# Kernel tuning notes

Hardware: AMD Instinct MI355X
Metric: run time of the kernel (lower is better)

Reference implementation:

```python
import jax, jax.numpy as jnp
import numpy as np

N, F_IN, E, H, C, B = 50000, 128, 800000, 64, 10, 512


def gcn_conv(x, W, b, src, dst, n):
    # PyG GCNConv: h = xW; add self-loops; norm = d^-1/2[src]*d^-1/2[dst]; scatter-add; + bias
    h = x @ W
    deg = jax.ops.segment_sum(jnp.ones(src.shape[0], h.dtype), dst, num_segments=n) + 1.0  # +1 self-loop
    dinv = jax.lax.rsqrt(deg)
    msg = h[src] * (dinv[src] * dinv[dst])[:, None]            # [E, H] gather + scale
    out = jax.ops.segment_sum(msg, dst, num_segments=n)        # scatter-add over targets
    out = out + h * (dinv * dinv)[:, None]                      # self-loop term (norm = 1/deg)
    return out + b


def setup_inputs() -> dict:
    key = jax.random.key(0)
    ks = jax.random.split(key, 12)
    x = jax.random.normal(ks[0], (N, F_IN), dtype=jnp.float32)
    edge_index = jax.random.randint(ks[1], (2, E), 0, N)
    batch = jnp.sort(jax.random.randint(ks[2], (N,), 0, B))
    def glorot(k, fan_in, fan_out):
        s = np.sqrt(6.0 / (fan_in + fan_out)).astype(np.float32)
        return jax.random.uniform(k, (fan_in, fan_out), jnp.float32, -s, s)
    return {
        "x": x, "edge_index": edge_index, "batch": batch,
        "W1": glorot(ks[3], F_IN, H), "b1": jnp.zeros((H,), jnp.float32),
        "W2": glorot(ks[4], H, H),    "b2": jnp.zeros((H,), jnp.float32),
        "W3": glorot(ks[5], H, H),    "b3": jnp.zeros((H,), jnp.float32),
        "Wl": glorot(ks[6], H, C),    "bl": jnp.zeros((C,), jnp.float32),
    }


def reference(x, edge_index, batch, W1, b1, W2, b2, W3, b3, Wl, bl):
    src, dst = edge_index[0], edge_index[1]
    n = x.shape[0]
    h = jax.nn.relu(gcn_conv(x, W1, b1, src, dst, n))
    h = jax.nn.relu(gcn_conv(h, W2, b2, src, dst, n))
    h = gcn_conv(h, W3, b3, src, dst, n)
    # global mean pool over graphs
    sums = jax.ops.segment_sum(h, batch, num_segments=B)
    cnts = jax.ops.segment_sum(jnp.ones((n,), h.dtype), batch, num_segments=B)
    pooled = sums / jnp.maximum(cnts, 1.0)[:, None]
    # dropout is identity in eval mode
    return pooled @ Wl + bl
```

## Files before the change

### kernel.cpp

```cpp
#include <hip/hip_runtime.h>

#define NBSHIFT 8
#define MAXB    5120
#define CHUNK   4096
#define TPB     256

__device__ inline unsigned short f2bf(float f) {
    unsigned u = __builtin_bit_cast(unsigned, f);
    unsigned r = u + 0x7FFFu + ((u >> 16) & 1u);
    return (unsigned short)(r >> 16);
}
__device__ inline float bflo(unsigned u) { return __builtin_bit_cast(float, u << 16); }
__device__ inline float bfhi(unsigned u) { return __builtin_bit_cast(float, u & 0xFFFF0000u); }

__global__ void k_init(int* __restrict__ bcur, int NB) {
    int t = threadIdx.x;
    if (t < NB) bcur[t] = 0;
}

__global__ __launch_bounds__(TPB) void k_bin_seg(const int* __restrict__ src,
                                                 const int* __restrict__ dst,
                                                 int* __restrict__ bcur,
                                                 unsigned* __restrict__ pairbuf,
                                                 const int* __restrict__ batch,
                                                 int* __restrict__ segs,
                                                 int* __restrict__ sege,
                                                 int E, int N, int B, int NB,
                                                 int nbChunk) {
    __shared__ int sdst[CHUNK];
    __shared__ int lcnt[256];
    __shared__ int lbase[256];
    int t = threadIdx.x;
    if ((int)blockIdx.x < nbChunk) {
        int e0 = blockIdx.x * CHUNK;
        int n = min(e0 + CHUNK, E) - e0;
        lcnt[t] = 0;
        __syncthreads();
        for (int i = t; i < n; i += TPB) {
            int d = dst[e0 + i];
            sdst[i] = d;
            atomicAdd(&lcnt[d >> NBSHIFT], 1);
        }
        __syncthreads();
        if (t < NB) {
            int c = lcnt[t];
            lbase[t] = c ? atomicAdd(&bcur[t], c) : 0;
            lcnt[t] = 0;
        }
        __syncthreads();
        for (int i = t; i < n; i += TPB) {
            int d = sdst[i];
            int b = d >> NBSHIFT;
            int pos = lbase[b] + atomicAdd(&lcnt[b], 1);
            pairbuf[(size_t)b * MAXB + pos] =
                ((unsigned)(d & 255) << 24) | (unsigned)src[e0 + i];
        }
    } else {
        int g = ((int)blockIdx.x - nbChunk) * TPB + t;
        if (g < B) {
            int lo = 0, hi = N;
            while (lo < hi) { int m = (lo + hi) >> 1; if (batch[m] < g) lo = m + 1; else hi = m; }
            int s = lo;
            lo = s; hi = N;
            while (lo < hi) { int m = (lo + hi) >> 1; if (batch[m] < g + 1) lo = m + 1; else hi = m; }
            segs[g] = s;
            sege[g] = lo;
        }
    }
}

template <int KHALVES>
__device__ void gemm_tile(const float* __restrict__ in, const float* __restrict__ W,
                          const float* __restrict__ sc, unsigned short* __restrict__ outb,
                          int tile, int N, float* sf) {
    float* sX = sf;
    float* sW = sf + 4096;
    const int K = KHALVES * 64;
    int t = threadIdx.x, w = t >> 6, l = t & 63;
    int node0 = tile * 64;
    int fg = l & 15, ngl = w * 4 + (l >> 4);
    float4 a0 = make_float4(0.f, 0.f, 0.f, 0.f), a1 = a0, a2 = a0, a3 = a0;

    for (int h = 0; h < KHALVES; ++h) {
        __syncthreads();
        for (int i = t; i < 64 * 16; i += TPB)
            ((float4*)sW)[i] = ((const float4*)(W + h * 64 * 64))[i];
        {
            int node = node0 + l;
            bool ok = node < N;
            const float* rp = in + (size_t)node * K + h * 64;
            for (int k0 = w * 16; k0 < w * 16 + 16; k0 += 4) {
                float4 v = ok ? *(const float4*)(rp + k0) : make_float4(0.f, 0.f, 0.f, 0.f);
                sX[(k0 + 0) * 64 + l] = v.x;
                sX[(k0 + 1) * 64 + l] = v.y;
                sX[(k0 + 2) * 64 + l] = v.z;
                sX[(k0 + 3) * 64 + l] = v.w;
            }
        }
        __syncthreads();
#pragma unroll 8
        for (int k = 0; k < 64; ++k) {
            float4 xv = *(const float4*)(sX + k * 64 + ngl * 4);
            float4 wv = *(const float4*)(sW + k * 64 + fg * 4);
            a0.x += xv.x * wv.x; a0.y += xv.x * wv.y; a0.z += xv.x * wv.z; a0.w += xv.x * wv.w;
            a1.x += xv.y * wv.x; a1.y += xv.y * wv.y; a1.z += xv.y * wv.z; a1.w += xv.y * wv.w;
            a2.x += xv.z * wv.x; a2.y += xv.z * wv.y; a2.z += xv.z * wv.z; a2.w += xv.z * wv.w;
            a3.x += xv.w * wv.x; a3.y += xv.w * wv.y; a3.z += xv.w * wv.z; a3.w += xv.w * wv.w;
        }
    }
    int nbase = node0 + ngl * 4;
    float4 accs[4] = {a0, a1, a2, a3};
#pragma unroll
    for (int i = 0; i < 4; ++i) {
        int n = nbase + i;
        if (n < N) {
            float s = sc ? sc[n] : 1.0f;
            float4 o = accs[i];
            ushort4 ob;
            ob.x = f2bf(o.x * s); ob.y = f2bf(o.y * s);
            ob.z = f2bf(o.z * s); ob.w = f2bf(o.w * s);
            *(ushort4*)(outb + (size_t)n * 64 + fg * 4) = ob;
        }
    }
}

__global__ __launch_bounds__(TPB) void k_build_gemm1(const unsigned* __restrict__ pairbuf,
                                                     const int* __restrict__ bcur,
                                                     int* __restrict__ pofs,
                                                     float* __restrict__ dinv,
                                                     int* __restrict__ ssrc,
                                                     const float* __restrict__ x,
                                                     const float* __restrict__ W1,
                                                     unsigned short* __restrict__ hsb,
                                                     int N, int NB) {
    __shared__ __align__(16) float sf[8192];
    int* si = (int*)sf;
    int t = threadIdx.x;
    int bid = blockIdx.x;
    if (bid < NB) {
        int* hcnt = si;
        int* sd   = si + 256;
        int* hcur = si + 512;
        size_t s0 = (size_t)bid * MAXB;
        int cb = bcur[bid];
        hcnt[t] = 0;
        __syncthreads();
        for (int i = t; i < cb; i += TPB)
            atomicAdd(&hcnt[pairbuf[s0 + i] >> 24], 1);
        __syncthreads();
        int c = hcnt[t];
        sd[t] = c;
        __syncthreads();
        int sum = c;
        for (int d = 1; d < 256; d <<= 1) {
            int a = (t >= d) ? sd[t - d] : 0;
            __syncthreads();
            sum += a; sd[t] = sum;
            __syncthreads();
        }
        int excl = sum - c;
        int node = (bid << NBSHIFT) + t;
        if (node < N) {
            pofs[node] = (excl << 8) | c;
            dinv[node] = rsqrtf((float)c + 1.0f);
        }
        hcur[t] = excl;
        __syncthreads();
        for (int i = t; i < cb; i += TPB) {
            unsigned p = pairbuf[s0 + i];
            int pos = atomicAdd(&hcur[p >> 24], 1);
            ssrc[s0 + pos] = (int)(p & 0x00FFFFFFu);
        }
    } else {
        gemm_tile<2>(x, W1, nullptr, hsb, bid - NB, N, sf);
    }
}

template <bool EDGEDINV, bool RELU>
__device__ float4 agg_row(const unsigned short* __restrict__ hs,
                          const int* __restrict__ ssrc, const int* __restrict__ pofs,
                          const float* __restrict__ dinv, const float* __restrict__ bias,
                          int v) {
    int lane = threadIdx.x & 63, g = lane >> 4, fl = lane & 15;
    int pk = pofs[v];
    size_t start = (size_t)(v >> NBSHIFT) * MAXB + (pk >> 8);
    int cnt = pk & 255;
    float dv = dinv[v];
    float4 acc = make_float4(0.f, 0.f, 0.f, 0.f);
#define BF_ACCS(p, s)                                                          \
    do {                                                                       \
        acc.x += bflo((p).x) * (s); acc.y += bfhi((p).x) * (s);                \
        acc.z += bflo((p).y) * (s); acc.w += bfhi((p).y) * (s);                \
    } while (0)
    if (g == 0) {
        uint2 p = *(const uint2*)(hs + (size_t)v * 64 + fl * 4);
        float sc = EDGEDINV ? dv : 1.0f;
        BF_ACCS(p, sc);
    }
    int j = 0, cnt16 = cnt & ~15;
    for (; j < cnt16; j += 16) {
        int s0 = ssrc[start + j + g];
        int s1 = ssrc[start + j + 4 + g];
        int s2 = ssrc[start + j + 8 + g];
        int s3 = ssrc[start + j + 12 + g];
        float d0 = 1.f, d1 = 1.f, d2 = 1.f, d3 = 1.f;
        if (EDGEDINV) { d0 = dinv[s0]; d1 = dinv[s1]; d2 = dinv[s2]; d3 = dinv[s3]; }
        uint2 h0 = *(const uint2*)(hs + (size_t)s0 * 64 + fl * 4);
        uint2 h1 = *(const uint2*)(hs + (size_t)s1 * 64 + fl * 4);
        uint2 h2 = *(const uint2*)(hs + (size_t)s2 * 64 + fl * 4);
        uint2 h3 = *(const uint2*)(hs + (size_t)s3 * 64 + fl * 4);
        BF_ACCS(h0, d0); BF_ACCS(h1, d1); BF_ACCS(h2, d2); BF_ACCS(h3, d3);
    }
    int cnt4 = cnt & ~3;
    for (; j < cnt4; j += 4) {
        int s = ssrc[start + j + g];
        float d = EDGEDINV ? dinv[s] : 1.f;
        uint2 h = *(const uint2*)(hs + (size_t)s * 64 + fl * 4);
        BF_ACCS(h, d);
    }
    int rem = cnt - cnt4;
    if (g < rem) {
        int s = ssrc[start + cnt4 + g];
        float d = EDGEDINV ? dinv[s] : 1.f;
        uint2 h = *(const uint2*)(hs + (size_t)s * 64 + fl * 4);
        BF_ACCS(h, d);
    }
#undef BF_ACCS
    acc.x += __shfl_xor(acc.x, 16); acc.y += __shfl_xor(acc.y, 16);
    acc.z += __shfl_xor(acc.z, 16); acc.w += __shfl_xor(acc.w, 16);
    acc.x += __shfl_xor(acc.x, 32); acc.y += __shfl_xor(acc.y, 32);
    acc.z += __shfl_xor(acc.z, 32); acc.w += __shfl_xor(acc.w, 32);
    float4 bv = *(const float4*)(bias + fl * 4);
    float4 o;
    o.x = acc.x * dv + bv.x; o.y = acc.y * dv + bv.y;
    o.z = acc.z * dv + bv.z; o.w = acc.w * dv + bv.w;
    if (RELU) {
        o.x = fmaxf(o.x, 0.f); o.y = fmaxf(o.y, 0.f);
        o.z = fmaxf(o.z, 0.f); o.w = fmaxf(o.w, 0.f);
    }
    return o;
}

template <bool EDGEDINV>
__global__ __launch_bounds__(512) void k_agg_gemm_tile(const unsigned short* __restrict__ hs,
                                                       const int* __restrict__ ssrc,
                                                       const int* __restrict__ pofs,
                                                       const float* __restrict__ dinv,
                                                       const float* __restrict__ bias,
                                                       const float* __restrict__ W,
                                                       unsigned short* __restrict__ outb,
                                                       int N) {
    __shared__ float sX[64 * 64];
    __shared__ float sW[64 * 64];
    int t = threadIdx.x, w = t >> 6, l = t & 63;
    int g = l >> 4, fl = l & 15;
    for (int i = t; i < 64 * 16; i += 512)
        ((float4*)sW)[i] = ((const float4*)W)[i];
    int node0 = blockIdx.x * 64;
#pragma unroll 2
    for (int i = 0; i < 8; ++i) {
        int nl = w * 8 + i;
        int v = node0 + nl;
        if (v < N) {
            float4 row = agg_row<EDGEDINV, true>(hs, ssrc, pofs, dinv, bias, v);
            if (g == 0) {
                sX[(fl * 4 + 0) * 64 + nl] = row.x;
                sX[(fl * 4 + 1) * 64 + nl] = row.y;
                sX[(fl * 4 + 2) * 64 + nl] = row.z;
                sX[(fl * 4 + 3) * 64 + nl] = row.w;
            }
        }
    }
    __syncthreads();
    int ng = w * 4 + g;
    float4 a0 = make_float4(0.f, 0.f, 0.f, 0.f), a1 = a0;
#pragma unroll 8
    for (int k = 0; k < 64; ++k) {
        float2 xv = *(const float2*)(sX + k * 64 + ng * 2);
        float4 wv = *(const float4*)(sW + k * 64 + fl * 4);
        a0.x += xv.x * wv.x; a0.y += xv.x * wv.y; a0.z += xv.x * wv.z; a0.w += xv.x * wv.w;
        a1.x += xv.y * wv.x; a1.y += xv.y * wv.y; a1.z += xv.y * wv.z; a1.w += xv.y * wv.w;
    }
    int n0 = node0 + ng * 2;
    if (n0 < N) {
        float s = dinv[n0];
        ushort4 ob;
        ob.x = f2bf(a0.x * s); ob.y = f2bf(a0.y * s);
        ob.z = f2bf(a0.z * s); ob.w = f2bf(a0.w * s);
        *(ushort4*)(outb + (size_t)n0 * 64 + fl * 4) = ob;
    }
    if (n0 + 1 < N) {
        float s = dinv[n0 + 1];
        ushort4 ob;
        ob.x = f2bf(a1.x * s); ob.y = f2bf(a1.y * s);
        ob.z = f2bf(a1.z * s); ob.w = f2bf(a1.w * s);
        *(ushort4*)(outb + (size_t)(n0 + 1) * 64 + fl * 4) = ob;
    }
}

__global__ __launch_bounds__(TPB) void k_agg3(const unsigned short* __restrict__ hs,
                                              const int* __restrict__ ssrc,
                                              const int* __restrict__ pofs,
                                              const float* __restrict__ dinv,
                                              const float* __restrict__ bias,
                                              float* __restrict__ outp, int N) {
    int t = threadIdx.x;
    int wave = t >> 6, lane = t & 63;
    int g = lane >> 4, fl = lane & 15;
    int v = blockIdx.x * 4 + wave;
    if (v >= N) return;
    float4 o = agg_row<false, false>(hs, ssrc, pofs, dinv, bias, v);
    if (g == 0)
        *(float4*)(outp + (size_t)v * 64 + fl * 4) = o;
}

__global__ __launch_bounds__(64) void k_pool_classify(const float* __restrict__ h,
                                                      const int* __restrict__ ss,
                                                      const int* __restrict__ se,
                                                      const float* __restrict__ Wl,
                                                      const float* __restrict__ bl,
                                                      float* __restrict__ out, int C) {
    int b = blockIdx.x;
    int lane = threadIdx.x;
    int g = lane >> 4, fl = lane & 15;
    int s = ss[b], e = se[b];
    float4 acc = make_float4(0.f, 0.f, 0.f, 0.f);
#pragma unroll 2
    for (int v = s + g; v < e; v += 4) {
        float4 hv = *(const float4*)(h + (size_t)v * 64 + fl * 4);
        acc.x += hv.x; acc.y += hv.y; acc.z += hv.z; acc.w += hv.w;
    }
    acc.x += __shfl_xor(acc.x, 16); acc.y += __shfl_xor(acc.y, 16);
    acc.z += __shfl_xor(acc.z, 16); acc.w += __shfl_xor(acc.w, 16);
    acc.x += __shfl_xor(acc.x, 32); acc.y += __shfl_xor(acc.y, 32);
    acc.z += __shfl_xor(acc.z, 32); acc.w += __shfl_xor(acc.w, 32);
    if (g == 0) {
        int cnt = e - s;
        if (cnt < 1) cnt = 1;
        float inv = 1.0f / (float)cnt;
        float4 p;
        p.x = acc.x * inv; p.y = acc.y * inv; p.z = acc.z * inv; p.w = acc.w * inv;
        int f0 = fl * 4;
        for (int c = 0; c < C; ++c) {
            float tt = p.x * Wl[(f0 + 0) * C + c] + p.y * Wl[(f0 + 1) * C + c]
                     + p.z * Wl[(f0 + 2) * C + c] + p.w * Wl[(f0 + 3) * C + c];
            tt += __shfl_xor(tt, 1); tt += __shfl_xor(tt, 2);
            tt += __shfl_xor(tt, 4); tt += __shfl_xor(tt, 8);
            if (fl == 0) out[b * C + c] = tt + bl[c];
        }
    }
}


extern "C" void kernel_launch(void* const* d_in, const int* in_sizes, int n_in,
                              void* d_out, int out_size, void* d_ws, size_t ws_size,
                              hipStream_t stream) {
    const float* x    = (const float*)d_in[0];
    const int*   ei   = (const int*)d_in[1];
    const int*   batch= (const int*)d_in[2];
    const float* W1   = (const float*)d_in[3];
    const float* b1   = (const float*)d_in[4];
    const float* W2   = (const float*)d_in[5];
    const float* b2   = (const float*)d_in[6];
    const float* W3   = (const float*)d_in[7];
    const float* b3   = (const float*)d_in[8];
    const float* Wl   = (const float*)d_in[9];
    const float* bl   = (const float*)d_in[10];
    float* out = (float*)d_out;

    const int N = in_sizes[2];
    const int E = in_sizes[1] / 2;
    const int C = 10;
    const int B = out_size / C;
    const int NB = (N + (1 << NBSHIFT) - 1) >> NBSHIFT;
    const int nbChunk = (E + CHUNK - 1) / CHUNK;
    const int nbSeg = (B + TPB - 1) / TPB;
    const int ntiles = (N + 63) / 64;

    char* ws = (char*)d_ws;
    auto alloc = [&](size_t bytes) {
        char* p = ws;
        ws += (bytes + 255) & ~(size_t)255;
        return p;
    };
    int*   bcur = (int*)alloc((size_t)NB * 4);
    int*   segs = (int*)alloc((size_t)B * 4);
    int*   sege = (int*)alloc((size_t)B * 4);
    int*   pofs = (int*)alloc((size_t)N * 4);
    float* dinv = (float*)alloc((size_t)N * 4);
    int*   ssrc = (int*)alloc((size_t)NB * MAXB * 4);
    unsigned short* hsb  = (unsigned short*)alloc((size_t)N * 64 * 2);
    unsigned short* hsb2 = (unsigned short*)alloc((size_t)N * 64 * 2);
    float* act  = (float*)alloc((size_t)N * 64 * 4);
    unsigned* pairbuf = (unsigned*)act;

    const int* src = ei;
    const int* dst = ei + E;

    int gAgg = (N + 3) / 4;

    k_init<<<1, TPB, 0, stream>>>(bcur, NB);
    k_bin_seg<<<nbChunk + nbSeg, TPB, 0, stream>>>(src, dst, bcur, pairbuf,
                                                   batch, segs, sege, E, N, B, NB, nbChunk);
    k_build_gemm1<<<NB + ntiles, TPB, 0, stream>>>(pairbuf, bcur, pofs, dinv, ssrc,
                                                   x, W1, hsb, N, NB);
    k_agg_gemm_tile<true><<<ntiles, 512, 0, stream>>>(hsb, ssrc, pofs, dinv, b1, W2, hsb2, N);
    k_agg_gemm_tile<false><<<ntiles, 512, 0, stream>>>(hsb2, ssrc, pofs, dinv, b2, W3, hsb, N);
    k_agg3<<<gAgg, TPB, 0, stream>>>(hsb, ssrc, pofs, dinv, b3, act, N);
    k_pool_classify<<<B, 64, 0, stream>>>(act, segs, sege, Wl, bl, out, C);
}
```

Baseline: 150.7 us.

## Fuse final aggregation with mean-pool via atomics and shrink binning chunk

The third-layer aggregation is fused with graph pooling. Each wave aggregates 8 consecutive nodes, accumulates rows belonging to the same graph, and atomically adds partial sums into a zeroed pooled buffer. This removes the N×64 fp32 activation write and its re-read by a separate pool kernel, and a small head kernel then does the classifier. The edge-binning chunk size also drops from 4096 to 1024 to launch more blocks, and pairbuf gets its own allocation instead of aliasing the activation buffer. In exchange, the fused path adds float atomic contention and makes the pooled sums order-nondeterministic.

```diff
diff --git a/kernel.cpp b/kernel.cpp
--- a/kernel.cpp
+++ b/kernel.cpp
@@ -2,7 +2,7 @@
 
 #define NBSHIFT 8
 #define MAXB    5120
-#define CHUNK   4096
+#define CHUNK   1024
 #define TPB     256
 
 __device__ inline unsigned short f2bf(float f) {
@@ -13,9 +13,14 @@
 __device__ inline float bflo(unsigned u) { return __builtin_bit_cast(float, u << 16); }
 __device__ inline float bfhi(unsigned u) { return __builtin_bit_cast(float, u & 0xFFFF0000u); }
 
-__global__ void k_init(int* __restrict__ bcur, int NB) {
-    int t = threadIdx.x;
-    if (t < NB) bcur[t] = 0;
+__global__ void k_init(int* __restrict__ bcur, float* __restrict__ pooled,
+                       int NB, int PF) {
+    int bid = blockIdx.x, t = threadIdx.x;
+    if (bid == 0 && t < NB) bcur[t] = 0;
+    if (bid >= 1) {
+        int i = (bid - 1) * TPB + t;
+        if (i < PF) pooled[i] = 0.f;
+    }
 }
 
 __global__ __launch_bounds__(TPB) void k_bin_seg(const int* __restrict__ src,
@@ -298,56 +303,58 @@
     }
 }
 
-__global__ __launch_bounds__(TPB) void k_agg3(const unsigned short* __restrict__ hs,
-                                              const int* __restrict__ ssrc,
-                                              const int* __restrict__ pofs,
-                                              const float* __restrict__ dinv,
-                                              const float* __restrict__ bias,
-                                              float* __restrict__ outp, int N) {
-    int t = threadIdx.x;
-    int wave = t >> 6, lane = t & 63;
-    int g = lane >> 4, fl = lane & 15;
-    int v = blockIdx.x * 4 + wave;
-    if (v >= N) return;
-    float4 o = agg_row<false, false>(hs, ssrc, pofs, dinv, bias, v);
-    if (g == 0)
-        *(float4*)(outp + (size_t)v * 64 + fl * 4) = o;
-}
-
-__global__ __launch_bounds__(64) void k_pool_classify(const float* __restrict__ h,
-                                                      const int* __restrict__ ss,
-                                                      const int* __restrict__ se,
-                                                      const float* __restrict__ Wl,
-                                                      const float* __restrict__ bl,
-                                                      float* __restrict__ out, int C) {
-    int b = blockIdx.x;
-    int lane = threadIdx.x;
-    int g = lane >> 4, fl = lane & 15;
-    int s = ss[b], e = se[b];
-    float4 acc = make_float4(0.f, 0.f, 0.f, 0.f);
-#pragma unroll 2
-    for (int v = s + g; v < e; v += 4) {
-        float4 hv = *(const float4*)(h + (size_t)v * 64 + fl * 4);
-        acc.x += hv.x; acc.y += hv.y; acc.z += hv.z; acc.w += hv.w;
-    }
-    acc.x += __shfl_xor(acc.x, 16); acc.y += __shfl_xor(acc.y, 16);
-    acc.z += __shfl_xor(acc.z, 16); acc.w += __shfl_xor(acc.w, 16);
-    acc.x += __shfl_xor(acc.x, 32); acc.y += __shfl_xor(acc.y, 32);
-    acc.z += __shfl_xor(acc.z, 32); acc.w += __shfl_xor(acc.w, 32);
-    if (g == 0) {
-        int cnt = e - s;
-        if (cnt < 1) cnt = 1;
-        float inv = 1.0f / (float)cnt;
-        float4 p;
-        p.x = acc.x * inv; p.y = acc.y * inv; p.z = acc.z * inv; p.w = acc.w * inv;
-        int f0 = fl * 4;
-        for (int c = 0; c < C; ++c) {
-            float tt = p.x * Wl[(f0 + 0) * C + c] + p.y * Wl[(f0 + 1) * C + c]
-                     + p.z * Wl[(f0 + 2) * C + c] + p.w * Wl[(f0 + 3) * C + c];
-            tt += __shfl_xor(tt, 1); tt += __shfl_xor(tt, 2);
-            tt += __shfl_xor(tt, 4); tt += __shfl_xor(tt, 8);
-            if (fl == 0) out[b * C + c] = tt + bl[c];
-        }
+__global__ __launch_bounds__(512) void k_agg3_pool(const unsigned short* __restrict__ hs,
+                                                   const int* __restrict__ ssrc,
+                                                   const int* __restrict__ pofs,
+                                                   const float* __restrict__ dinv,
+                                                   const float* __restrict__ bias,
+                                                   const int* __restrict__ batch,
+                                                   float* __restrict__ pooled, int N) {
+    int t = threadIdx.x, w = t >> 6, l = t & 63;
+    int g = l >> 4;
+    int node0 = blockIdx.x * 64 + w * 8;
+    float4 pacc = make_float4(0.f, 0.f, 0.f, 0.f);
+    int curg = -1;
+    for (int i = 0; i < 8; ++i) {
+        int v = node0 + i;
+        if (v >= N) break;
+        float4 row = agg_row<false, false>(hs, ssrc, pofs, dinv, bias, v);
+        int gid = batch[v];
+        if (gid != curg) {
+            if (curg >= 0) {
+                float comp = (g == 0) ? pacc.x : (g == 1) ? pacc.y : (g == 2) ? pacc.z : pacc.w;
+                atomicAdd(&pooled[curg * 64 + (l & 15) * 4 + g], comp);
+            }
+            curg = gid;
+            pacc = row;
+        } else {
+            pacc.x += row.x; pacc.y += row.y; pacc.z += row.z; pacc.w += row.w;
+        }
+    }
+    if (curg >= 0) {
+        float comp = (g == 0) ? pacc.x : (g == 1) ? pacc.y : (g == 2) ? pacc.z : pacc.w;
+        atomicAdd(&pooled[curg * 64 + (l & 15) * 4 + g], comp);
+    }
+}
+
+__global__ __launch_bounds__(TPB) void k_head(const float* __restrict__ pooled,
+                                              const int* __restrict__ ss,
+                                              const int* __restrict__ se,
+                                              const float* __restrict__ Wl,
+                                              const float* __restrict__ bl,
+                                              float* __restrict__ out, int B, int C) {
+    int t = threadIdx.x, w = t >> 6, l = t & 63;
+    int b = blockIdx.x * 4 + w;
+    if (b >= B) return;
+    int cnt = se[b] - ss[b];
+    if (cnt < 1) cnt = 1;
+    float p = pooled[b * 64 + l] / (float)cnt;
+    for (int c = 0; c < C; ++c) {
+        float tt = p * Wl[l * C + c];
+        tt += __shfl_xor(tt, 1);  tt += __shfl_xor(tt, 2);
+        tt += __shfl_xor(tt, 4);  tt += __shfl_xor(tt, 8);
+        tt += __shfl_xor(tt, 16); tt += __shfl_xor(tt, 32);
+        if (l == 0) out[b * C + c] = tt + bl[c];
     }
 }
 
@@ -376,6 +383,7 @@
     const int nbChunk = (E + CHUNK - 1) / CHUNK;
     const int nbSeg = (B + TPB - 1) / TPB;
     const int ntiles = (N + 63) / 64;
+    const int PF = B * 64;
 
     char* ws = (char*)d_ws;
     auto alloc = [&](size_t bytes) {
@@ -383,29 +391,27 @@
         ws += (bytes + 255) & ~(size_t)255;
         return p;
     };
-    int*   bcur = (int*)alloc((size_t)NB * 4);
-    int*   segs = (int*)alloc((size_t)B * 4);
-    int*   sege = (int*)alloc((size_t)B * 4);
-    int*   pofs = (int*)alloc((size_t)N * 4);
-    float* dinv = (float*)alloc((size_t)N * 4);
-    int*   ssrc = (int*)alloc((size_t)NB * MAXB * 4);
+    int*   bcur   = (int*)alloc((size_t)NB * 4);
+    int*   segs   = (int*)alloc((size_t)B * 4);
+    int*   sege   = (int*)alloc((size_t)B * 4);
+    int*   pofs   = (int*)alloc((size_t)N * 4);
+    float* dinv   = (float*)alloc((size_t)N * 4);
+    float* pooled = (float*)alloc((size_t)PF * 4);
+    int*   ssrc   = (int*)alloc((size_t)NB * MAXB * 4);
+    unsigned* pairbuf = (unsigned*)alloc((size_t)NB * MAXB * 4);
     unsigned short* hsb  = (unsigned short*)alloc((size_t)N * 64 * 2);
     unsigned short* hsb2 = (unsigned short*)alloc((size_t)N * 64 * 2);
-    float* act  = (float*)alloc((size_t)N * 64 * 4);
-    unsigned* pairbuf = (unsigned*)act;
 
     const int* src = ei;
     const int* dst = ei + E;
 
-    int gAgg = (N + 3) / 4;
-
-    k_init<<<1, TPB, 0, stream>>>(bcur, NB);
+    k_init<<<1 + (PF + TPB - 1) / TPB, TPB, 0, stream>>>(bcur, pooled, NB, PF);
     k_bin_seg<<<nbChunk + nbSeg, TPB, 0, stream>>>(src, dst, bcur, pairbuf,
                                                    batch, segs, sege, E, N, B, NB, nbChunk);
     k_build_gemm1<<<NB + ntiles, TPB, 0, stream>>>(pairbuf, bcur, pofs, dinv, ssrc,
                                                    x, W1, hsb, N, NB);
     k_agg_gemm_tile<true><<<ntiles, 512, 0, stream>>>(hsb, ssrc, pofs, dinv, b1, W2, hsb2, N);
     k_agg_gemm_tile<false><<<ntiles, 512, 0, stream>>>(hsb2, ssrc, pofs, dinv, b2, W3, hsb, N);
-    k_agg3<<<gAgg, TPB, 0, stream>>>(hsb, ssrc, pofs, dinv, b3, act, N);
-    k_pool_classify<<<B, 64, 0, stream>>>(act, segs, sege, Wl, bl, out, C);
-}
+    k_agg3_pool<<<ntiles, 512, 0, stream>>>(hsb, ssrc, pofs, dinv, b3, batch, pooled, N);
+    k_head<<<(B + 3) / 4, TPB, 0, stream>>>(pooled, segs, sege, Wl, bl, out, B, C);
+}
```

Result: slower. 157.1 us (+4.2%).
